# Optimization experiments

Measured on AMD Instinct MI355X. Metric: run time of the kernel, lower is better.

The kernel has to match this reference:

```python
import jax, jax.numpy as jnp
import numpy as np

B, L, H, FUTURE = 256, 1000, 51, 100


def setup_inputs() -> dict:
    key = jax.random.key(0)
    ks = jax.random.split(key, 11)
    s = 1.0 / np.sqrt(H)
    return {
        "x": jax.random.normal(ks[0], (B, L), dtype=jnp.float32),
        "W_ih1": jax.random.uniform(ks[1], (4 * H, 1), jnp.float32, -s, s),
        "W_hh1": jax.random.uniform(ks[2], (4 * H, H), jnp.float32, -s, s),
        "b_ih1": jax.random.uniform(ks[3], (4 * H,), jnp.float32, -s, s),
        "b_hh1": jax.random.uniform(ks[4], (4 * H,), jnp.float32, -s, s),
        "W_ih2": jax.random.uniform(ks[5], (4 * H, H), jnp.float32, -s, s),
        "W_hh2": jax.random.uniform(ks[6], (4 * H, H), jnp.float32, -s, s),
        "b_ih2": jax.random.uniform(ks[7], (4 * H,), jnp.float32, -s, s),
        "b_hh2": jax.random.uniform(ks[8], (4 * H,), jnp.float32, -s, s),
        "W_lin": jax.random.uniform(ks[9], (1, H), jnp.float32, -s, s),
        "b_lin": jax.random.uniform(ks[10], (1,), jnp.float32, -s, s),
        "future": FUTURE,
    }


def _lstm_cell(x_t, h, c, W_ih, W_hh, b):
    # PyTorch LSTMCell gate order: i, f, g, o
    gates = x_t @ W_ih.T + h @ W_hh.T + b  # [B, 4H]
    i, f, g, o = jnp.split(gates, 4, axis=-1)
    c_new = jax.nn.sigmoid(f) * c + jax.nn.sigmoid(i) * jnp.tanh(g)
    h_new = jax.nn.sigmoid(o) * jnp.tanh(c_new)
    return h_new, c_new


def reference(x, W_ih1, W_hh1, b_ih1, b_hh1, W_ih2, W_hh2, b_ih2, b_hh2,
              W_lin, b_lin, future):
    b1 = b_ih1 + b_hh1
    b2 = b_ih2 + b_hh2
    n, hs = x.shape[0], W_hh1.shape[1]
    zeros = jnp.zeros((n, hs), dtype=x.dtype)

    def cell_step(carry, x_t):
        h1, c1, h2, c2 = carry
        h1, c1 = _lstm_cell(x_t, h1, c1, W_ih1, W_hh1, b1)
        h2, c2 = _lstm_cell(h1, h2, c2, W_ih2, W_hh2, b2)
        out = h2 @ W_lin.T + b_lin  # [B, 1]
        return (h1, c1, h2, c2), out

    xs = x.T[:, :, None]  # [L, B, 1]
    carry, outs_seq = jax.lax.scan(cell_step, (zeros, zeros, zeros, zeros), xs)

    def future_step(carry, _):
        h1, c1, h2, c2, out = carry
        (h1, c1, h2, c2), new_out = cell_step((h1, c1, h2, c2), out)
        return (h1, c1, h2, c2, new_out), new_out

    last = outs_seq[-1]
    _, outs_fut = jax.lax.scan(future_step, (*carry, last), None, length=future)

    outs = jnp.concatenate([outs_seq, outs_fut], axis=0)  # [L+F, B, 1]
    return outs[:, :, 0].T  # [B, L+F]
```

## Files before the change

### kernel.cpp

```cpp
#include <hip/hip_runtime.h>


#define B_   256
#define L_   1000
#define H_   51
#define HP   64
#define G4   204
#define GP   208
#define T_   1100

__device__ __forceinline__ float frcp(float v) { return __builtin_amdgcn_rcpf(v); }
__device__ __forceinline__ float sigf(float v) {
    return frcp(1.0f + __expf(-v));
}
__device__ __forceinline__ float tanh_fast(float v) {
    float a = fminf(fmaxf(v, -9.0f), 9.0f);
    float e = __expf(2.0f * a);
    return (e - 1.0f) * frcp(e + 1.0f);
}

#define RLF(k, acc) acc = fmaf(__int_as_float(__builtin_amdgcn_readlane(vhi, k)), wr##k, acc)

#define MATVEC() do { \
    float a0 = bias, a1 = 0.f, a2 = 0.f, a3 = 0.f; \
    RLF(0,a0);  RLF(1,a1);  RLF(2,a2);  RLF(3,a3); \
    RLF(4,a0);  RLF(5,a1);  RLF(6,a2);  RLF(7,a3); \
    RLF(8,a0);  RLF(9,a1);  RLF(10,a2); RLF(11,a3); \
    RLF(12,a0); RLF(13,a1); RLF(14,a2); RLF(15,a3); \
    RLF(16,a0); RLF(17,a1); RLF(18,a2); RLF(19,a3); \
    RLF(20,a0); RLF(21,a1); RLF(22,a2); RLF(23,a3); \
    RLF(24,a0); RLF(25,a1); RLF(26,a2); RLF(27,a3); \
    RLF(28,a0); RLF(29,a1); RLF(30,a2); RLF(31,a3); \
    RLF(32,a0); RLF(33,a1); RLF(34,a2); RLF(35,a3); \
    RLF(36,a0); RLF(37,a1); RLF(38,a2); RLF(39,a3); \
    RLF(40,a0); RLF(41,a1); RLF(42,a2); RLF(43,a3); \
    RLF(44,a0); RLF(45,a1); RLF(46,a2); RLF(47,a3); \
    RLF(48,a0); RLF(49,a1); RLF(50,a2); \
    gdst[0] = (a0 + a1) + (a2 + a3); } while (0)

__attribute__((amdgpu_flat_work_group_size(768, 768), amdgpu_waves_per_eu(3, 3)))
__global__ void lstm_pred_kernel(const float* __restrict__ x,
                      const float* __restrict__ W_ih1, const float* __restrict__ W_hh1,
                      const float* __restrict__ b_ih1, const float* __restrict__ b_hh1,
                      const float* __restrict__ W_ih2, const float* __restrict__ W_hh2,
                      const float* __restrict__ b_ih2, const float* __restrict__ b_hh2,
                      const float* __restrict__ W_lin, const float* __restrict__ b_lin,
                      float* __restrict__ out)
{
    __shared__ float xrow[L_];
    __shared__ alignas(16) float gall[3 * GP];
    __shared__ alignas(16) float hs0[HP];
    __shared__ alignas(16) float hs1[HP];
    __shared__ float out_s;

    const int tid  = threadIdx.x;
    const int b    = blockIdx.x;
    const int g    = tid >> 8;
    const int j    = tid & 255;
    const int lane = tid & 63;
    const bool act = (j < G4);

    for (int i = tid; i < L_; i += 768) xrow[i] = x[(size_t)b * L_ + i];
    if (tid < HP) { hs0[tid] = 0.0f; hs1[tid] = 0.0f; }

    const float* wrow = (g == 0) ? (W_hh1 + j * H_)
                      : (g == 1) ? (W_ih2 + j * H_)
                                 : (W_hh2 + j * H_);
    float bias = 0.0f;
    float wr0=0.f,wr1=0.f,wr2=0.f,wr3=0.f,wr4=0.f,wr5=0.f,wr6=0.f,wr7=0.f,
          wr8=0.f,wr9=0.f,wr10=0.f,wr11=0.f,wr12=0.f,wr13=0.f,wr14=0.f,wr15=0.f,
          wr16=0.f,wr17=0.f,wr18=0.f,wr19=0.f,wr20=0.f,wr21=0.f,wr22=0.f,wr23=0.f,
          wr24=0.f,wr25=0.f,wr26=0.f,wr27=0.f,wr28=0.f,wr29=0.f,wr30=0.f,wr31=0.f,
          wr32=0.f,wr33=0.f,wr34=0.f,wr35=0.f,wr36=0.f,wr37=0.f,wr38=0.f,wr39=0.f,
          wr40=0.f,wr41=0.f,wr42=0.f,wr43=0.f,wr44=0.f,wr45=0.f,wr46=0.f,wr47=0.f,
          wr48=0.f,wr49=0.f,wr50=0.f;
    if (act) {
        if (g == 0)      bias = b_ih1[j] + b_hh1[j];
        else if (g == 1) bias = b_ih2[j] + b_hh2[j];
        wr0 =wrow[0];  wr1 =wrow[1];  wr2 =wrow[2];  wr3 =wrow[3];
        wr4 =wrow[4];  wr5 =wrow[5];  wr6 =wrow[6];  wr7 =wrow[7];
        wr8 =wrow[8];  wr9 =wrow[9];  wr10=wrow[10]; wr11=wrow[11];
        wr12=wrow[12]; wr13=wrow[13]; wr14=wrow[14]; wr15=wrow[15];
        wr16=wrow[16]; wr17=wrow[17]; wr18=wrow[18]; wr19=wrow[19];
        wr20=wrow[20]; wr21=wrow[21]; wr22=wrow[22]; wr23=wrow[23];
        wr24=wrow[24]; wr25=wrow[25]; wr26=wrow[26]; wr27=wrow[27];
        wr28=wrow[28]; wr29=wrow[29]; wr30=wrow[30]; wr31=wrow[31];
        wr32=wrow[32]; wr33=wrow[33]; wr34=wrow[34]; wr35=wrow[35];
        wr36=wrow[36]; wr37=wrow[37]; wr38=wrow[38]; wr39=wrow[39];
        wr40=wrow[40]; wr41=wrow[41]; wr42=wrow[42]; wr43=wrow[43];
        wr44=wrow[44]; wr45=wrow[45]; wr46=wrow[46]; wr47=wrow[47];
        wr48=wrow[48]; wr49=wrow[49]; wr50=wrow[50];
    }
    asm volatile("" :
        "+v"(wr0),"+v"(wr1),"+v"(wr2),"+v"(wr3),"+v"(wr4),"+v"(wr5),"+v"(wr6),
        "+v"(wr7),"+v"(wr8),"+v"(wr9),"+v"(wr10),"+v"(wr11),"+v"(wr12),"+v"(wr13),
        "+v"(wr14),"+v"(wr15),"+v"(wr16),"+v"(wr17),"+v"(wr18),"+v"(wr19),
        "+v"(wr20),"+v"(wr21),"+v"(wr22),"+v"(wr23),"+v"(wr24),"+v"(wr25));
    asm volatile("" :
        "+v"(wr26),"+v"(wr27),"+v"(wr28),"+v"(wr29),"+v"(wr30),"+v"(wr31),
        "+v"(wr32),"+v"(wr33),"+v"(wr34),"+v"(wr35),"+v"(wr36),"+v"(wr37),
        "+v"(wr38),"+v"(wr39),"+v"(wr40),"+v"(wr41),"+v"(wr42),"+v"(wr43),
        "+v"(wr44),"+v"(wr45),"+v"(wr46),"+v"(wr47),"+v"(wr48),"+v"(wr49),
        "+v"(wr50),"+v"(bias));
    float* gdst = gall + g * GP + j;
    const float* hsrc = (g == 2) ? hs1 : hs0;

    float wi0 = 0.f, wi1 = 0.f, wi2 = 0.f, wi3 = 0.f, wlin = 0.f;
    if (tid < H_) {
        wi0 = W_ih1[tid];
        wi1 = W_ih1[tid + H_];
        wi2 = W_ih1[tid + 2 * H_];
        wi3 = W_ih1[tid + 3 * H_];
    }
    if (tid >= 256 && tid < 256 + H_) wlin = W_lin[tid - 256];
    const float blin = b_lin[0];

    float c1 = 0.f, c2 = 0.f;
    float* outp = out + (size_t)b * T_;

    if (g == 0 && act) gall[j] = bias;
    __syncthreads();
    if (tid < H_) {
        const float xv = xrow[0];
        float gi = fmaf(wi0, xv, gall[tid]);
        float gf = fmaf(wi1, xv, gall[tid + H_]);
        float gg = fmaf(wi2, xv, gall[tid + 2 * H_]);
        float go = fmaf(wi3, xv, gall[tid + 3 * H_]);
        float ig = sigf(gi), fg = sigf(gf), gv = tanh_fast(gg), og = sigf(go);
        c1 = fmaf(fg, c1, ig * gv);
        hs0[tid] = og * tanh_fast(c1);
    }
    __syncthreads();

    for (int t = 0; t < L_ - 1; ++t) {
        const int vhi = __float_as_int(hsrc[lane]);
        if (act) MATVEC();
        __syncthreads();

        if (tid >= 256 && tid < 320) {
            float p = 0.f;
            const int q2 = tid - 256;
            if (q2 < H_) {
                float gi = gall[GP + q2]        + gall[2*GP + q2];
                float gf = gall[GP + q2 +   H_] + gall[2*GP + q2 +   H_];
                float gg = gall[GP + q2 + 2*H_] + gall[2*GP + q2 + 2*H_];
                float go = gall[GP + q2 + 3*H_] + gall[2*GP + q2 + 3*H_];
                float ig = sigf(gi), fg = sigf(gf), gv = tanh_fast(gg), og = sigf(go);
                c2 = fmaf(fg, c2, ig * gv);
                float h2n = og * tanh_fast(c2);
                hs1[q2] = h2n;
                p = h2n * wlin;
            }
#pragma unroll
            for (int off = 32; off > 0; off >>= 1) p += __shfl_down(p, off);
            if (q2 == 0) outp[t] = p + blin;
        }
        if (tid < H_) {
            const float xv = xrow[t + 1];
            float gi = fmaf(wi0, xv, gall[tid]);
            float gf = fmaf(wi1, xv, gall[tid + H_]);
            float gg = fmaf(wi2, xv, gall[tid + 2 * H_]);
            float go = fmaf(wi3, xv, gall[tid + 3 * H_]);
            float ig = sigf(gi), fg = sigf(gf), gv = tanh_fast(gg), og = sigf(go);
            c1 = fmaf(fg, c1, ig * gv);
            hs0[tid] = og * tanh_fast(c1);
        }
        __syncthreads();
    }

    for (int t = L_ - 1; t < T_; ++t) {
        const int vhi = __float_as_int(hsrc[lane]);
        if (act) MATVEC();
        __syncthreads();

        if (tid >= 256 && tid < 320) {
            float p = 0.f;
            const int q2 = tid - 256;
            if (q2 < H_) {
                float gi = gall[GP + q2]        + gall[2*GP + q2];
                float gf = gall[GP + q2 +   H_] + gall[2*GP + q2 +   H_];
                float gg = gall[GP + q2 + 2*H_] + gall[2*GP + q2 + 2*H_];
                float go = gall[GP + q2 + 3*H_] + gall[2*GP + q2 + 3*H_];
                float ig = sigf(gi), fg = sigf(gf), gv = tanh_fast(gg), og = sigf(go);
                c2 = fmaf(fg, c2, ig * gv);
                float h2n = og * tanh_fast(c2);
                hs1[q2] = h2n;
                p = h2n * wlin;
            }
#pragma unroll
            for (int off = 32; off > 0; off >>= 1) p += __shfl_down(p, off);
            if (q2 == 0) { float o = p + blin; out_s = o; outp[t] = o; }
        }
        __syncthreads();

        if (tid < H_) {
            const float xv = out_s;
            float gi = fmaf(wi0, xv, gall[tid]);
            float gf = fmaf(wi1, xv, gall[tid + H_]);
            float gg = fmaf(wi2, xv, gall[tid + 2 * H_]);
            float go = fmaf(wi3, xv, gall[tid + 3 * H_]);
            float ig = sigf(gi), fg = sigf(gf), gv = tanh_fast(gg), og = sigf(go);
            c1 = fmaf(fg, c1, ig * gv);
            hs0[tid] = og * tanh_fast(c1);
        }
        __syncthreads();
    }
}

extern "C" void kernel_launch(void* const* d_in, const int* in_sizes, int n_in,
                              void* d_out, int out_size, void* d_ws, size_t ws_size,
                              hipStream_t stream)
{
    const float* x     = (const float*)d_in[0];
    const float* W_ih1 = (const float*)d_in[1];
    const float* W_hh1 = (const float*)d_in[2];
    const float* b_ih1 = (const float*)d_in[3];
    const float* b_hh1 = (const float*)d_in[4];
    const float* W_ih2 = (const float*)d_in[5];
    const float* W_hh2 = (const float*)d_in[6];
    const float* b_ih2 = (const float*)d_in[7];
    const float* b_hh2 = (const float*)d_in[8];
    const float* W_lin = (const float*)d_in[9];
    const float* b_lin = (const float*)d_in[10];
    float* out = (float*)d_out;

    lstm_pred_kernel<<<B_, 768, 0, stream>>>(x, W_ih1, W_hh1, b_ih1, b_hh1,
                                             W_ih2, W_hh2, b_ih2, b_hh2,
                                             W_lin, b_lin, out);
}
```

Baseline: 1.091 ms.

## Keep LSTM hidden state in registers, interleave gate rows, double-buffer gates

Weight rows are reordered so each hidden unit's four gates sit contiguously, which lets one float4 LDS read fetch them. Every wave now computes the cell update redundantly and keeps h in a register. That register is read directly by readlane in the matvec, so the shared h arrays and their round trips go away. Gate buffers are double-buffered, which cuts the teacher-forced phase to one barrier per step. The costs are redundant activation math across waves and a reliance on the lane-to-unit mapping.

```diff
diff --git a/kernel.cpp b/kernel.cpp
--- a/kernel.cpp
+++ b/kernel.cpp
@@ -4,9 +4,6 @@
 #define B_   256
 #define L_   1000
 #define H_   51
-#define HP   64
-#define G4   204
-#define GP   208
 #define T_   1100
 
 __device__ __forceinline__ float frcp(float v) { return __builtin_amdgcn_rcpf(v); }
@@ -21,7 +18,8 @@
 
 #define RLF(k, acc) acc = fmaf(__int_as_float(__builtin_amdgcn_readlane(vhi, k)), wr##k, acc)
 
-#define MATVEC() do { \
+#define MATVEC(dst) do { \
+    const int vhi = __float_as_int(hl); \
     float a0 = bias, a1 = 0.f, a2 = 0.f, a3 = 0.f; \
     RLF(0,a0);  RLF(1,a1);  RLF(2,a2);  RLF(3,a3); \
     RLF(4,a0);  RLF(5,a1);  RLF(6,a2);  RLF(7,a3); \
@@ -36,7 +34,7 @@
     RLF(40,a0); RLF(41,a1); RLF(42,a2); RLF(43,a3); \
     RLF(44,a0); RLF(45,a1); RLF(46,a2); RLF(47,a3); \
     RLF(48,a0); RLF(49,a1); RLF(50,a2); \
-    gdst[0] = (a0 + a1) + (a2 + a3); } while (0)
+    (dst) = (a0 + a1) + (a2 + a3); } while (0)
 
 __attribute__((amdgpu_flat_work_group_size(768, 768), amdgpu_waves_per_eu(3, 3)))
 __global__ void lstm_pred_kernel(const float* __restrict__ x,
@@ -48,24 +46,22 @@
                       float* __restrict__ out)
 {
     __shared__ float xrow[L_];
-    __shared__ alignas(16) float gall[3 * GP];
-    __shared__ alignas(16) float hs0[HP];
-    __shared__ alignas(16) float hs1[HP];
+    __shared__ alignas(16) float gbuf[2][3][256];
     __shared__ float out_s;
 
     const int tid  = threadIdx.x;
     const int b    = blockIdx.x;
-    const int g    = tid >> 8;
+    const int lane = tid & 63;
+    const int wv   = tid >> 6;
+    const int grp  = tid >> 8;
     const int j    = tid & 255;
-    const int lane = tid & 63;
-    const bool act = (j < G4);
+    const bool act = (j < 204);
 
     for (int i = tid; i < L_; i += 768) xrow[i] = x[(size_t)b * L_ + i];
-    if (tid < HP) { hs0[tid] = 0.0f; hs1[tid] = 0.0f; }
 
-    const float* wrow = (g == 0) ? (W_hh1 + j * H_)
-                      : (g == 1) ? (W_ih2 + j * H_)
-                                 : (W_hh2 + j * H_);
+    const int r = (j & 3) * H_ + (j >> 2);
+    const float* Wsrc = (grp == 0) ? W_hh1 : (grp == 1) ? W_ih2 : W_hh2;
+    const float* wrow = Wsrc + r * H_;
     float bias = 0.0f;
     float wr0=0.f,wr1=0.f,wr2=0.f,wr3=0.f,wr4=0.f,wr5=0.f,wr6=0.f,wr7=0.f,
           wr8=0.f,wr9=0.f,wr10=0.f,wr11=0.f,wr12=0.f,wr13=0.f,wr14=0.f,wr15=0.f,
@@ -75,8 +71,8 @@
           wr40=0.f,wr41=0.f,wr42=0.f,wr43=0.f,wr44=0.f,wr45=0.f,wr46=0.f,wr47=0.f,
           wr48=0.f,wr49=0.f,wr50=0.f;
     if (act) {
-        if (g == 0)      bias = b_ih1[j] + b_hh1[j];
-        else if (g == 1) bias = b_ih2[j] + b_hh2[j];
+        if (grp == 0)      bias = b_ih1[r] + b_hh1[r];
+        else if (grp == 1) bias = b_ih2[r] + b_hh2[r];
         wr0 =wrow[0];  wr1 =wrow[1];  wr2 =wrow[2];  wr3 =wrow[3];
         wr4 =wrow[4];  wr5 =wrow[5];  wr6 =wrow[6];  wr7 =wrow[7];
         wr8 =wrow[8];  wr9 =wrow[9];  wr10=wrow[10]; wr11=wrow[11];
@@ -102,108 +98,68 @@
         "+v"(wr38),"+v"(wr39),"+v"(wr40),"+v"(wr41),"+v"(wr42),"+v"(wr43),
         "+v"(wr44),"+v"(wr45),"+v"(wr46),"+v"(wr47),"+v"(wr48),"+v"(wr49),
         "+v"(wr50),"+v"(bias));
-    float* gdst = gall + g * GP + j;
-    const float* hsrc = (g == 2) ? hs1 : hs0;
 
-    float wi0 = 0.f, wi1 = 0.f, wi2 = 0.f, wi3 = 0.f, wlin = 0.f;
-    if (tid < H_) {
-        wi0 = W_ih1[tid];
-        wi1 = W_ih1[tid + H_];
-        wi2 = W_ih1[tid + 2 * H_];
-        wi3 = W_ih1[tid + 3 * H_];
+    float wiu0=0.f, wiu1=0.f, wiu2=0.f, wiu3=0.f, wl=0.f;
+    if (grp < 2) {
+        if (lane < H_) {
+            wiu0 = W_ih1[lane];
+            wiu1 = W_ih1[lane + H_];
+            wiu2 = W_ih1[lane + 2 * H_];
+            wiu3 = W_ih1[lane + 3 * H_];
+        }
+    } else {
+        if (lane < H_) wl = W_lin[lane];
     }
-    if (tid >= 256 && tid < 256 + H_) wlin = W_lin[tid - 256];
     const float blin = b_lin[0];
-
-    float c1 = 0.f, c2 = 0.f;
+    float hl = 0.0f, cl = 0.0f;
     float* outp = out + (size_t)b * T_;
 
-    if (g == 0 && act) gall[j] = bias;
-    __syncthreads();
-    if (tid < H_) {
-        const float xv = xrow[0];
-        float gi = fmaf(wi0, xv, gall[tid]);
-        float gf = fmaf(wi1, xv, gall[tid + H_]);
-        float gg = fmaf(wi2, xv, gall[tid + 2 * H_]);
-        float go = fmaf(wi3, xv, gall[tid + 3 * H_]);
-        float ig = sigf(gi), fg = sigf(gf), gv = tanh_fast(gg), og = sigf(go);
-        c1 = fmaf(fg, c1, ig * gv);
-        hs0[tid] = og * tanh_fast(c1);
-    }
+    if (grp == 0 && act) gbuf[0][0][j] = bias;
     __syncthreads();
 
-    for (int t = 0; t < L_ - 1; ++t) {
-        const int vhi = __float_as_int(hsrc[lane]);
-        if (act) MATVEC();
-        __syncthreads();
+    int p = 0;
+    for (int t = 0; t <= T_; ++t) {
+        const bool fut = (t >= L_);
 
-        if (tid >= 256 && tid < 320) {
-            float p = 0.f;
-            const int q2 = tid - 256;
-            if (q2 < H_) {
-                float gi = gall[GP + q2]        + gall[2*GP + q2];
-                float gf = gall[GP + q2 +   H_] + gall[2*GP + q2 +   H_];
-                float gg = gall[GP + q2 + 2*H_] + gall[2*GP + q2 + 2*H_];
-                float go = gall[GP + q2 + 3*H_] + gall[2*GP + q2 + 3*H_];
-                float ig = sigf(gi), fg = sigf(gf), gv = tanh_fast(gg), og = sigf(go);
-                c2 = fmaf(fg, c2, ig * gv);
-                float h2n = og * tanh_fast(c2);
-                hs1[q2] = h2n;
-                p = h2n * wlin;
+        if (grp == 2 && t > 0) {
+            const float4 ga = *(const float4*)&gbuf[p][1][4 * lane];
+            const float4 gb = *(const float4*)&gbuf[p][2][4 * lane];
+            float ig = sigf(ga.x + gb.x);
+            float fg = sigf(ga.y + gb.y);
+            float gv = tanh_fast(ga.z + gb.z);
+            float og = sigf(ga.w + gb.w);
+            cl = fmaf(fg, cl, ig * gv);
+            hl = og * tanh_fast(cl);
+            if (wv == 8) {
+                float pp = (lane < H_) ? hl * wl : 0.0f;
+#pragma unroll
+                for (int off = 32; off > 0; off >>= 1) pp += __shfl_down(pp, off);
+                if (lane == 0) {
+                    float o = pp + blin;
+                    outp[t - 1] = o;
+                    if (fut) out_s = o;
+                }
             }
-#pragma unroll
-            for (int off = 32; off > 0; off >>= 1) p += __shfl_down(p, off);
-            if (q2 == 0) outp[t] = p + blin;
         }
-        if (tid < H_) {
-            const float xv = xrow[t + 1];
-            float gi = fmaf(wi0, xv, gall[tid]);
-            float gf = fmaf(wi1, xv, gall[tid + H_]);
-            float gg = fmaf(wi2, xv, gall[tid + 2 * H_]);
-            float go = fmaf(wi3, xv, gall[tid + 3 * H_]);
-            float ig = sigf(gi), fg = sigf(gf), gv = tanh_fast(gg), og = sigf(go);
-            c1 = fmaf(fg, c1, ig * gv);
-            hs0[tid] = og * tanh_fast(c1);
+
+        if (fut) __syncthreads();
+
+        if (grp < 2 && t < T_) {
+            const float4 g1 = *(const float4*)&gbuf[p][0][4 * lane];
+            const float xv = fut ? out_s : xrow[t];
+            float ig = sigf(fmaf(wiu0, xv, g1.x));
+            float fg = sigf(fmaf(wiu1, xv, g1.y));
+            float gv = tanh_fast(fmaf(wiu2, xv, g1.z));
+            float og = sigf(fmaf(wiu3, xv, g1.w));
+            cl = fmaf(fg, cl, ig * gv);
+            hl = og * tanh_fast(cl);
+        }
+
+        if (t < T_ && act) {
+            MATVEC(gbuf[p ^ 1][grp][j]);
         }
         __syncthreads();
-    }
-
-    for (int t = L_ - 1; t < T_; ++t) {
-        const int vhi = __float_as_int(hsrc[lane]);
-        if (act) MATVEC();
-        __syncthreads();
-
-        if (tid >= 256 && tid < 320) {
-            float p = 0.f;
-            const int q2 = tid - 256;
-            if (q2 < H_) {
-                float gi = gall[GP + q2]        + gall[2*GP + q2];
-                float gf = gall[GP + q2 +   H_] + gall[2*GP + q2 +   H_];
-                float gg = gall[GP + q2 + 2*H_] + gall[2*GP + q2 + 2*H_];
-                float go = gall[GP + q2 + 3*H_] + gall[2*GP + q2 + 3*H_];
-                float ig = sigf(gi), fg = sigf(gf), gv = tanh_fast(gg), og = sigf(go);
-                c2 = fmaf(fg, c2, ig * gv);
-                float h2n = og * tanh_fast(c2);
-                hs1[q2] = h2n;
-                p = h2n * wlin;
-            }
-#pragma unroll
-            for (int off = 32; off > 0; off >>= 1) p += __shfl_down(p, off);
-            if (q2 == 0) { float o = p + blin; out_s = o; outp[t] = o; }
-        }
-        __syncthreads();
-
-        if (tid < H_) {
-            const float xv = out_s;
-            float gi = fmaf(wi0, xv, gall[tid]);
-            float gf = fmaf(wi1, xv, gall[tid + H_]);
-            float gg = fmaf(wi2, xv, gall[tid + 2 * H_]);
-            float go = fmaf(wi3, xv, gall[tid + 3 * H_]);
-            float ig = sigf(gi), fg = sigf(gf), gv = tanh_fast(gg), og = sigf(go);
-            c1 = fmaf(fg, c1, ig * gv);
-            hs0[tid] = og * tanh_fast(c1);
-        }
-        __syncthreads();
+        p ^= 1;
     }
 }
 
```

After: 1.202 ms. +10.1%, slower.
